# Optimization experiments

Measured on AMD Instinct MI355X. Metric: run time of the kernel, lower is better.

## Reference

```python
import jax, jax.numpy as jnp
import numpy as np

N_NODES = 50000
N_EDGES = 800000
H_DIM = 64
N_RELS = 8
N_BASES = 2
N_LAYERS = 2


def setup_inputs() -> dict:
    key = jax.random.key(0)
    ks = jax.random.split(key, 10)
    scale = 1.0 / np.sqrt(H_DIM)
    features = jax.random.normal(ks[0], (N_NODES, H_DIM), dtype=jnp.float32)
    src = jax.random.randint(ks[1], (N_EDGES,), 0, N_NODES, dtype=jnp.int32)
    dst = jax.random.randint(ks[2], (N_EDGES,), 0, N_NODES, dtype=jnp.int32)
    etype = jax.random.randint(ks[3], (N_EDGES,), 0, N_RELS, dtype=jnp.int32)
    # basis weights V: [L, B, H, H], coefficients comp: [L, R, B]
    V = jax.random.normal(ks[4], (N_LAYERS, N_BASES, H_DIM, H_DIM), dtype=jnp.float32) * scale
    comp = jax.random.normal(ks[5], (N_LAYERS, N_RELS, N_BASES), dtype=jnp.float32)
    loop_w = jax.random.normal(ks[6], (N_LAYERS, H_DIM, H_DIM), dtype=jnp.float32) * scale
    layer_bias = jnp.zeros((N_LAYERS, H_DIM), dtype=jnp.float32)
    fc_w = jax.random.normal(ks[7], (1, N_NODES * H_DIM), dtype=jnp.float32) * (1.0 / np.sqrt(N_NODES * H_DIM))
    fc_b = jnp.zeros((1,), dtype=jnp.float32)
    return {
        "features": features, "V": V, "comp": comp, "loop_w": loop_w,
        "layer_bias": layer_bias, "fc_w": fc_w, "fc_b": fc_b,
        "src": src, "dst": dst, "etype": etype,
    }


def reference(features, V, comp, loop_w, layer_bias, fc_w, fc_b, src, dst, etype):
    N, H = features.shape
    L = V.shape[0]
    x = features
    for l in range(L):
        # basis decomposition: project nodes through each basis first (N*B*H, cheap),
        # then mix per-edge with relation coefficients -> avoids per-edge [H,H] weights
        proj = jnp.einsum('ni,bio->nbo', x, V[l])          # [N, B, H]
        msg = jnp.einsum('eb,ebo->eo', comp[l][etype], proj[src])  # [E, H]
        agg = jax.ops.segment_sum(msg, dst, num_segments=N)        # [N, H]
        h = agg + x @ loop_w[l] + layer_bias[l]
        x = jax.nn.relu(h) if l < L - 1 else h
    flat = x.reshape(1, -1)                                # [1, N*H]
    return jax.nn.sigmoid(flat @ fc_w.T + fc_b)            # [1, 1]
```

## Files before the change

### kernel.cpp

```cpp
#include <hip/hip_runtime.h>
#include <hip/hip_bf16.h>
#include <math.h>

#define N_NODES 50000
#define N_EDGES 800000
#define HDIM 64

#define NBUCKET 392
#define BSHIFT  7
#define NLOC    128
#define BCAP    3072

typedef short bf16x8 __attribute__((ext_vector_type(8)));
typedef float f32x4  __attribute__((ext_vector_type(4)));
typedef unsigned short ushort_t;

__device__ __forceinline__ ushort_t f2bf(float f) {
    __hip_bfloat16 b = __float2bfloat16(f);
    return *(ushort_t*)&b;
}

__global__ __launch_bounds__(256) void prep_kernel(
    const float* __restrict__ features, ushort_t* __restrict__ x_bf,
    const float* __restrict__ V, const float* __restrict__ lw,
    ushort_t* __restrict__ Wt, int* __restrict__ bucketFill,
    float* __restrict__ scalar, int* __restrict__ done)
{
    const int b = blockIdx.x;
    const int t = threadIdx.x;
    if (b < 3125) {
        const int i = b * 256 + t;
        const float4 v = ((const float4*)features)[i];
        ushort4 o = { f2bf(v.x), f2bf(v.y), f2bf(v.z), f2bf(v.w) };
        *(ushort4*)&x_bf[(size_t)i * 4] = o;
    } else if (b < 3221) {
        const int e = (b - 3125) * 256 + t;
        const int l = e / 12288, r = e % 12288;
        const int n = r / 192, k = r % 192;
        const int sel = k >> 6, i = k & 63;
        const float val = (sel < 2) ? V[l * 8192 + sel * 4096 + i * 64 + n]
                                    : lw[l * 4096 + i * 64 + n];
        Wt[e] = f2bf(val);
    } else {
        for (int i = t; i < NBUCKET; i += 256) bucketFill[i] = 0;
        if (t == 0) { scalar[0] = 0.0f; done[0] = 0; }
    }
}

__global__ __launch_bounds__(256) void bucket_scatter(
    const int* __restrict__ src, const int* __restrict__ dst,
    const int* __restrict__ etype, int* __restrict__ bucketFill,
    unsigned int* __restrict__ buf)
{
    __shared__ int cnt[NBUCKET];
    __shared__ int base[NBUCKET];
    const int t = threadIdx.x;
    for (int i = t; i < NBUCKET; i += 256) cnt[i] = 0;
    __syncthreads();

    int rank[8], bkt[8];
    unsigned pay[8];
    bool valid[8];
#pragma unroll
    for (int k = 0; k < 8; ++k) {
        const int e = blockIdx.x * 2048 + k * 256 + t;
        valid[k] = (e < N_EDGES);
        if (valid[k]) {
            const int d = dst[e];
            const int b = d >> BSHIFT;
            bkt[k] = b;
            pay[k] = (unsigned)src[e] | ((unsigned)etype[e] << 16)
                   | ((unsigned)(d & (NLOC - 1)) << 19);
            rank[k] = atomicAdd(&cnt[b], 1);
        }
    }
    __syncthreads();
    for (int i = t; i < NBUCKET; i += 256)
        base[i] = atomicAdd(&bucketFill[i], cnt[i]);
    __syncthreads();
#pragma unroll
    for (int k = 0; k < 8; ++k) {
        if (valid[k]) {
            const int pos = base[bkt[k]] + rank[k];
            if (pos < BCAP) buf[bkt[k] * BCAP + pos] = pay[k];
        }
    }
}

__global__ __launch_bounds__(256) void bucket_sort(
    const unsigned int* __restrict__ buf, const int* __restrict__ bucketFill,
    unsigned int* __restrict__ edges, int* __restrict__ row_ptr)
{
    __shared__ int hist[NLOC];
    __shared__ int lscan[NLOC];
    __shared__ int cnt2[NLOC];
    __shared__ int sraw[448];
    __shared__ int sexc[448];
    const int b = blockIdx.x;
    const int t = threadIdx.x;

    if (t < NLOC) { hist[t] = 0; cnt2[t] = 0; }
    for (int i = t; i < 448; i += 256)
        sraw[i] = (i < NBUCKET) ? bucketFill[i] : 0;
    __syncthreads();

    if (t < 64) {
        int carry = 0;
        for (int c = 0; c < 7; ++c) {
            const int h = sraw[c * 64 + t];
            int x = h;
#pragma unroll
            for (int off = 1; off < 64; off <<= 1) {
                int u = __shfl_up(x, off, 64);
                if (t >= off) x += u;
            }
            sexc[c * 64 + t] = carry + x - h;
            carry += __shfl(x, 63, 64);
        }
    }
    __syncthreads();
    const int cntb = min(sraw[b], BCAP);
    const int bb   = sexc[b];

    for (int i0 = t; i0 < cntb; i0 += 1024) {
        const bool v1 = i0 + 256 < cntb, v2 = i0 + 512 < cntb, v3 = i0 + 768 < cntb;
        const unsigned p0 = buf[b * BCAP + i0];
        unsigned p1 = 0, p2 = 0, p3 = 0;
        if (v1) p1 = buf[b * BCAP + i0 + 256];
        if (v2) p2 = buf[b * BCAP + i0 + 512];
        if (v3) p3 = buf[b * BCAP + i0 + 768];
        atomicAdd(&hist[p0 >> 19], 1);
        if (v1) atomicAdd(&hist[p1 >> 19], 1);
        if (v2) atomicAdd(&hist[p2 >> 19], 1);
        if (v3) atomicAdd(&hist[p3 >> 19], 1);
    }
    __syncthreads();

    if (t < 64) {
        int carry = 0;
        for (int c = 0; c < 2; ++c) {
            const int h = hist[c * 64 + t];
            int x = h;
#pragma unroll
            for (int off = 1; off < 64; off <<= 1) {
                int u = __shfl_up(x, off, 64);
                if (t >= off) x += u;
            }
            lscan[c * 64 + t] = carry + x - h;
            carry += __shfl(x, 63, 64);
        }
    }
    __syncthreads();

    const int n0 = b << BSHIFT;
    if (t < NLOC) {
        const int g = n0 + t;
        if (g < N_NODES) row_ptr[g] = bb + lscan[t];
    }
    if (b == NBUCKET - 1 && t == 0) row_ptr[N_NODES] = bb + cntb;

    for (int i0 = t; i0 < cntb; i0 += 1024) {
        const bool v1 = i0 + 256 < cntb, v2 = i0 + 512 < cntb, v3 = i0 + 768 < cntb;
        const unsigned p0 = buf[b * BCAP + i0];
        unsigned p1 = 0, p2 = 0, p3 = 0;
        if (v1) p1 = buf[b * BCAP + i0 + 256];
        if (v2) p2 = buf[b * BCAP + i0 + 512];
        if (v3) p3 = buf[b * BCAP + i0 + 768];
        {
            const int d = p0 >> 19;
            const int r = atomicAdd(&cnt2[d], 1);
            edges[bb + lscan[d] + r] = p0;
        }
        if (v1) { const int d = p1 >> 19; const int r = atomicAdd(&cnt2[d], 1);
                  edges[bb + lscan[d] + r] = p1; }
        if (v2) { const int d = p2 >> 19; const int r = atomicAdd(&cnt2[d], 1);
                  edges[bb + lscan[d] + r] = p2; }
        if (v3) { const int d = p3 >> 19; const int r = atomicAdd(&cnt2[d], 1);
                  edges[bb + lscan[d] + r] = p3; }
    }
}

__global__ __launch_bounds__(256) void aggregate_v4(
    const ushort_t* __restrict__ x,
    const unsigned int* __restrict__ edges,
    const int* __restrict__ row_ptr,
    const float* __restrict__ comp_l,
    ushort_t* __restrict__ y)
{
    __shared__ float scomp[16];
    const int t = threadIdx.x;
    if (t < 16) scomp[t] = comp_l[t];
    __syncthreads();

    const int lane = t & 63;
    const int wv   = t >> 6;
    const int g    = lane >> 4;
    const int fq   = lane & 15;
    const int n    = blockIdx.x * 16 + wv * 4 + g;

    const int beg = row_ptr[n];
    const int end = row_ptr[n + 1];

    float a0[4], a1[4];
#pragma unroll
    for (int i = 0; i < 4; ++i) { a0[i] = 0.f; a1[i] = 0.f; }

    for (int j = beg; j < end; j += 4) {
        unsigned p[4];
#pragma unroll
        for (int k = 0; k < 4; ++k) {
            const int e = j + k;
            p[k] = edges[(e < end) ? e : (end - 1)];
        }
        uint2 u[4];
#pragma unroll
        for (int k = 0; k < 4; ++k)
            u[k] = *(const uint2*)&x[(size_t)(p[k] & 0xFFFFu) * 64 + fq * 4];
        float2 c[4];
#pragma unroll
        for (int k = 0; k < 4; ++k) {
            c[k] = *(const float2*)&scomp[((p[k] >> 16) & 7u) * 2];
            if (j + k >= end) { c[k].x = 0.f; c[k].y = 0.f; }
        }
#pragma unroll
        for (int k = 0; k < 4; ++k) {
            const float f0 = __uint_as_float(u[k].x << 16);
            const float f1 = __uint_as_float(u[k].x & 0xFFFF0000u);
            const float f2 = __uint_as_float(u[k].y << 16);
            const float f3 = __uint_as_float(u[k].y & 0xFFFF0000u);
            a0[0] = fmaf(c[k].x, f0, a0[0]); a1[0] = fmaf(c[k].y, f0, a1[0]);
            a0[1] = fmaf(c[k].x, f1, a0[1]); a1[1] = fmaf(c[k].y, f1, a1[1]);
            a0[2] = fmaf(c[k].x, f2, a0[2]); a1[2] = fmaf(c[k].y, f2, a1[2]);
            a0[3] = fmaf(c[k].x, f3, a0[3]); a1[3] = fmaf(c[k].y, f3, a1[3]);
        }
    }

    ushort4 s0 = { f2bf(a0[0]), f2bf(a0[1]), f2bf(a0[2]), f2bf(a0[3]) };
    ushort4 s1 = { f2bf(a1[0]), f2bf(a1[1]), f2bf(a1[2]), f2bf(a1[3]) };
    *(ushort4*)&y[(size_t)n * 128 + fq * 4]      = s0;
    *(ushort4*)&y[(size_t)n * 128 + 64 + fq * 4] = s1;
}

template <bool FUSE>
__global__ __launch_bounds__(256) void mfma_transform(
    const ushort_t* __restrict__ y_bf,
    const ushort_t* __restrict__ x_bf,
    const ushort_t* __restrict__ Wt,
    const float* __restrict__ bias,
    const float* __restrict__ fcw,
    ushort_t* __restrict__ xout,
    float* __restrict__ scalar,
    const float* __restrict__ fcb,
    int* __restrict__ done,
    float* __restrict__ outp)
{
    __shared__ __align__(16) ushort_t su[64 * 200];
    __shared__ float sred[4];
    const int t = threadIdx.x;
    const int w = t >> 6;
    const int lane = t & 63;
    const int c16 = lane & 15;
    const int quad = lane >> 4;
    const int tile = blockIdx.x;

    bf16x8 wf[6];
#pragma unroll
    for (int kf = 0; kf < 6; ++kf)
        wf[kf] = *(const bf16x8*)&Wt[(w * 16 + c16) * 192 + kf * 32 + quad * 8];
    const float bv = bias[w * 16 + c16];

#pragma unroll
    for (int k = 0; k < 6; ++k) {
        const int cid = t + 256 * k;
        const int row = cid / 24;
        const int part = cid % 24;
        const int n = tile * 64 + row;
        uint4 v = {0u, 0u, 0u, 0u};
        if (n < N_NODES) {
            v = (part < 16) ? *(const uint4*)&y_bf[(size_t)n * 128 + part * 8]
                            : *(const uint4*)&x_bf[(size_t)n * 64 + (part - 16) * 8];
        }
        *(uint4*)&su[row * 200 + part * 8] = v;
    }
    __syncthreads();

    float fsum = 0.f;
#pragma unroll
    for (int mt = 0; mt < 4; ++mt) {
        f32x4 acc = {bv, bv, bv, bv};
#pragma unroll
        for (int kf = 0; kf < 6; ++kf) {
            const bf16x8 af =
                *(const bf16x8*)&su[(mt * 16 + c16) * 200 + kf * 32 + quad * 8];
            acc = __builtin_amdgcn_mfma_f32_16x16x32_bf16(af, wf[kf], acc, 0, 0, 0);
        }
        const int nodeb = tile * 64 + mt * 16 + quad * 4;
        if (FUSE) {
#pragma unroll
            for (int r = 0; r < 4; ++r) {
                const int n = nodeb + r;
                if (n < N_NODES)
                    fsum += acc[r] * fcw[(size_t)n * 64 + w * 16 + c16];
            }
        } else {
#pragma unroll
            for (int r = 0; r < 4; ++r) {
                const int n = nodeb + r;
                if (n < N_NODES)
                    xout[(size_t)n * 64 + w * 16 + c16] = f2bf(fmaxf(acc[r], 0.f));
            }
        }
    }

    if (FUSE) {
#pragma unroll
        for (int off = 32; off; off >>= 1) fsum += __shfl_down(fsum, off, 64);
        if (lane == 0) sred[w] = fsum;
        __syncthreads();
        if (t == 0) {
            atomicAdd(scalar, sred[0] + sred[1] + sred[2] + sred[3]);
            __threadfence();
            const int ticket = atomicAdd(done, 1);
            if (ticket == (int)gridDim.x - 1) {
                const float v = atomicAdd(scalar, 0.0f) + fcb[0];
                outp[0] = 1.0f / (1.0f + expf(-v));
            }
        }
    }
}

extern "C" void kernel_launch(void* const* d_in, const int* in_sizes, int n_in,
                              void* d_out, int out_size, void* d_ws, size_t ws_size,
                              hipStream_t stream)
{
    const float* features = (const float*)d_in[0];
    const float* V        = (const float*)d_in[1];
    const float* comp     = (const float*)d_in[2];
    const float* loop_w   = (const float*)d_in[3];
    const float* bias     = (const float*)d_in[4];
    const float* fc_w     = (const float*)d_in[5];
    const float* fc_b     = (const float*)d_in[6];
    const int*   src      = (const int*)d_in[7];
    const int*   dst      = (const int*)d_in[8];
    const int*   etype    = (const int*)d_in[9];
    float* out = (float*)d_out;

    char* ws = (char*)d_ws;
    ushort_t*     y_bf    = (ushort_t*)(ws);
    ushort_t*     x_bf    = (ushort_t*)(ws + 12800000);
    ushort_t*     x1_bf   = (ushort_t*)(ws + 19200000);
    ushort_t*     Wt      = (ushort_t*)(ws + 25600000);
    float*        scalar  = (float*)   (ws + 25649152);
    int*          done    = (int*)     (ws + 25649156);
    int*          bucketFill = (int*)  (ws + 25649280);
    int*          row_ptr = (int*)     (ws + 25650944);
    unsigned int* edges   = (unsigned int*)(ws + 25851008);
    unsigned int* buf     = (unsigned int*)(ws + 29051008);

    const int aggBlocks = N_NODES / 16;
    const int mtBlocks  = (N_NODES + 63) / 64;
    const int k1Blocks  = (N_EDGES + 2047) / 2048;

    prep_kernel<<<3222, 256, 0, stream>>>(features, x_bf, V, loop_w, Wt,
                                          bucketFill, scalar, done);
    bucket_scatter<<<k1Blocks, 256, 0, stream>>>(src, dst, etype, bucketFill, buf);
    bucket_sort<<<NBUCKET, 256, 0, stream>>>(buf, bucketFill, edges, row_ptr);

    aggregate_v4<<<aggBlocks, 256, 0, stream>>>(x_bf, edges, row_ptr, comp, y_bf);
    mfma_transform<false><<<mtBlocks, 256, 0, stream>>>(
        y_bf, x_bf, Wt, bias, nullptr, x1_bf, nullptr, nullptr, nullptr, nullptr);

    aggregate_v4<<<aggBlocks, 256, 0, stream>>>(x1_bf, edges, row_ptr, comp + 16, y_bf);
    mfma_transform<true><<<mtBlocks, 256, 0, stream>>>(
        y_bf, x1_bf, Wt + 12288, bias + 64, fc_w, nullptr, scalar, fc_b, done, out);
}
```

Before: 188.8 us.

## Halve transform tile rows, use atomic loads for gathers, widen sort histogram

The MFMA transform kernel now processes 32 nodes per block instead of 64, which doubles the block count and halves shared memory per block to improve occupancy and tail balance. The aggregate kernel's neighbor gathers become relaxed agent-scope 64-bit atomic loads, probably to change the cache policy or instruction form of the gather. The bucket sort histogram arrays grow to 512 entries with a longer scan, which does extra work without changing output since only 128 local slots are used. These ideas are unrelated and add risk of slower gathers or extra scan overhead.

```diff
diff --git a/kernel.cpp b/kernel.cpp
--- a/kernel.cpp
+++ b/kernel.cpp
@@ -91,15 +91,16 @@
     const unsigned int* __restrict__ buf, const int* __restrict__ bucketFill,
     unsigned int* __restrict__ edges, int* __restrict__ row_ptr)
 {
-    __shared__ int hist[NLOC];
-    __shared__ int lscan[NLOC];
-    __shared__ int cnt2[NLOC];
+    __shared__ int hist[512];
+    __shared__ int lscan[512];
+    __shared__ int cnt2[512];
     __shared__ int sraw[448];
     __shared__ int sexc[448];
     const int b = blockIdx.x;
     const int t = threadIdx.x;
 
-    if (t < NLOC) { hist[t] = 0; cnt2[t] = 0; }
+    hist[t] = 0; hist[t + 256] = 0;
+    cnt2[t] = 0; cnt2[t + 256] = 0;
     for (int i = t; i < 448; i += 256)
         sraw[i] = (i < NBUCKET) ? bucketFill[i] : 0;
     __syncthreads();
@@ -138,7 +139,7 @@
 
     if (t < 64) {
         int carry = 0;
-        for (int c = 0; c < 2; ++c) {
+        for (int c = 0; c < 8; ++c) {
             const int h = hist[c * 64 + t];
             int x = h;
 #pragma unroll
@@ -153,9 +154,9 @@
     __syncthreads();
 
     const int n0 = b << BSHIFT;
-    if (t < NLOC) {
-        const int g = n0 + t;
-        if (g < N_NODES) row_ptr[g] = bb + lscan[t];
+    for (int i = t; i < 512; i += 256) {
+        const int g = n0 + i;
+        if (i < NLOC && g < N_NODES) row_ptr[g] = bb + lscan[i];
     }
     if (b == NBUCKET - 1 && t == 0) row_ptr[N_NODES] = bb + cntb;
 
@@ -180,7 +181,7 @@
     }
 }
 
-__global__ __launch_bounds__(256) void aggregate_v4(
+__global__ __launch_bounds__(256) void aggregate_v9(
     const ushort_t* __restrict__ x,
     const unsigned int* __restrict__ edges,
     const int* __restrict__ row_ptr,
@@ -212,10 +213,12 @@
             const int e = j + k;
             p[k] = edges[(e < end) ? e : (end - 1)];
         }
-        uint2 u[4];
+        unsigned long long u[4];
 #pragma unroll
         for (int k = 0; k < 4; ++k)
-            u[k] = *(const uint2*)&x[(size_t)(p[k] & 0xFFFFu) * 64 + fq * 4];
+            u[k] = __hip_atomic_load(
+                (const unsigned long long*)&x[(size_t)(p[k] & 0xFFFFu) * 64 + fq * 4],
+                __ATOMIC_RELAXED, __HIP_MEMORY_SCOPE_AGENT);
         float2 c[4];
 #pragma unroll
         for (int k = 0; k < 4; ++k) {
@@ -224,10 +227,12 @@
         }
 #pragma unroll
         for (int k = 0; k < 4; ++k) {
-            const float f0 = __uint_as_float(u[k].x << 16);
-            const float f1 = __uint_as_float(u[k].x & 0xFFFF0000u);
-            const float f2 = __uint_as_float(u[k].y << 16);
-            const float f3 = __uint_as_float(u[k].y & 0xFFFF0000u);
+            const unsigned lo = (unsigned)u[k];
+            const unsigned hi = (unsigned)(u[k] >> 32);
+            const float f0 = __uint_as_float(lo << 16);
+            const float f1 = __uint_as_float(lo & 0xFFFF0000u);
+            const float f2 = __uint_as_float(hi << 16);
+            const float f3 = __uint_as_float(hi & 0xFFFF0000u);
             a0[0] = fmaf(c[k].x, f0, a0[0]); a1[0] = fmaf(c[k].y, f0, a1[0]);
             a0[1] = fmaf(c[k].x, f1, a0[1]); a1[1] = fmaf(c[k].y, f1, a1[1]);
             a0[2] = fmaf(c[k].x, f2, a0[2]); a1[2] = fmaf(c[k].y, f2, a1[2]);
@@ -254,7 +259,7 @@
     int* __restrict__ done,
     float* __restrict__ outp)
 {
-    __shared__ __align__(16) ushort_t su[64 * 200];
+    __shared__ __align__(16) ushort_t su[32 * 200];
     __shared__ float sred[4];
     const int t = threadIdx.x;
     const int w = t >> 6;
@@ -270,11 +275,11 @@
     const float bv = bias[w * 16 + c16];
 
 #pragma unroll
-    for (int k = 0; k < 6; ++k) {
+    for (int k = 0; k < 3; ++k) {
         const int cid = t + 256 * k;
         const int row = cid / 24;
         const int part = cid % 24;
-        const int n = tile * 64 + row;
+        const int n = tile * 32 + row;
         uint4 v = {0u, 0u, 0u, 0u};
         if (n < N_NODES) {
             v = (part < 16) ? *(const uint4*)&y_bf[(size_t)n * 128 + part * 8]
@@ -286,7 +291,7 @@
 
     float fsum = 0.f;
 #pragma unroll
-    for (int mt = 0; mt < 4; ++mt) {
+    for (int mt = 0; mt < 2; ++mt) {
         f32x4 acc = {bv, bv, bv, bv};
 #pragma unroll
         for (int kf = 0; kf < 6; ++kf) {
@@ -294,7 +299,7 @@
                 *(const bf16x8*)&su[(mt * 16 + c16) * 200 + kf * 32 + quad * 8];
             acc = __builtin_amdgcn_mfma_f32_16x16x32_bf16(af, wf[kf], acc, 0, 0, 0);
         }
-        const int nodeb = tile * 64 + mt * 16 + quad * 4;
+        const int nodeb = tile * 32 + mt * 16 + quad * 4;
         if (FUSE) {
 #pragma unroll
             for (int r = 0; r < 4; ++r) {
@@ -358,7 +363,7 @@
     unsigned int* buf     = (unsigned int*)(ws + 29051008);
 
     const int aggBlocks = N_NODES / 16;
-    const int mtBlocks  = (N_NODES + 63) / 64;
+    const int mtBlocks  = (N_NODES + 31) / 32;
     const int k1Blocks  = (N_EDGES + 2047) / 2048;
 
     prep_kernel<<<3222, 256, 0, stream>>>(features, x_bf, V, loop_w, Wt,
@@ -366,11 +371,11 @@
     bucket_scatter<<<k1Blocks, 256, 0, stream>>>(src, dst, etype, bucketFill, buf);
     bucket_sort<<<NBUCKET, 256, 0, stream>>>(buf, bucketFill, edges, row_ptr);
 
-    aggregate_v4<<<aggBlocks, 256, 0, stream>>>(x_bf, edges, row_ptr, comp, y_bf);
+    aggregate_v9<<<aggBlocks, 256, 0, stream>>>(x_bf, edges, row_ptr, comp, y_bf);
     mfma_transform<false><<<mtBlocks, 256, 0, stream>>>(
         y_bf, x_bf, Wt, bias, nullptr, x1_bf, nullptr, nullptr, nullptr, nullptr);
 
-    aggregate_v4<<<aggBlocks, 256, 0, stream>>>(x1_bf, edges, row_ptr, comp + 16, y_bf);
+    aggregate_v9<<<aggBlocks, 256, 0, stream>>>(x1_bf, edges, row_ptr, comp + 16, y_bf);
     mfma_transform<true><<<mtBlocks, 256, 0, stream>>>(
         y_bf, x1_bf, Wt + 12288, bias + 64, fc_w, nullptr, scalar, fc_b, done, out);
 }
```

Result: slower. 209.4 us (+10.9%).
